# Kernel optimization log

Measured on AMD Instinct MI355X. Metric: run time of the kernel, lower is better.

The kernel has to match this reference:

```python
import jax, jax.numpy as jnp
import numpy as np

N = 50000      # nodes
E = 800000     # edges
F_IN = 512     # input feature dim
H1 = 8         # heads layer 1
F_HID = 8      # per-head hidden dim (concat -> 64)
H2 = 1         # heads layer 2
NLAB = 64      # output classes
LRELU_SLOPE = 0.2


def setup_inputs() -> dict:
    key = jax.random.key(0)
    ks = jax.random.split(key, 9)
    inputs = jax.random.normal(ks[0], (N, F_IN), jnp.float32)
    src = jax.random.randint(ks[1], (E,), 0, N, dtype=jnp.int32)
    dst = jax.random.randint(ks[2], (E,), 0, N, dtype=jnp.int32)
    s1 = 1.0 / np.sqrt(F_IN)
    s2 = 1.0 / np.sqrt(H1 * F_HID)
    W1 = jax.random.normal(ks[3], (H1, F_IN, F_HID), jnp.float32) * s1
    a1_src = jax.random.normal(ks[4], (H1, F_HID), jnp.float32) * 0.1
    a1_dst = jax.random.normal(ks[5], (H1, F_HID), jnp.float32) * 0.1
    W2 = jax.random.normal(ks[6], (H2, H1 * F_HID, NLAB), jnp.float32) * s2
    a2_src = jax.random.normal(ks[7], (H2, NLAB), jnp.float32) * 0.1
    a2_dst = jax.random.normal(ks[8], (H2, NLAB), jnp.float32) * 0.1
    return {"inputs": inputs, "W1": W1, "a1_src": a1_src, "a1_dst": a1_dst,
            "W2": W2, "a2_src": a2_src, "a2_dst": a2_dst, "src": src, "dst": dst}


def gat_layer(x, W, a_s, a_d, src, dst):
    # x: [N, F]; W: [H, F, O]; a_s/a_d: [H, O]
    Wh = jnp.einsum('nf,hfo->nho', x, W)                    # [N, H, O]
    es = jnp.einsum('nho,ho->nh', Wh, a_s)                  # [N, H]
    ed = jnp.einsum('nho,ho->nh', Wh, a_d)                  # [N, H]
    e = jax.nn.leaky_relu(es[src] + ed[dst], LRELU_SLOPE)   # [E, H]
    # neighborhood softmax over incoming edges of each dst node
    m = jax.lax.stop_gradient(jax.ops.segment_max(e, dst, num_segments=N))
    ex = jnp.exp(e - m[dst])                                # [E, H]
    den = jax.ops.segment_sum(ex, dst, num_segments=N)      # [N, H]
    alpha = ex / (den[dst] + 1e-10)                         # [E, H]
    msgs = alpha[:, :, None] * Wh[src]                      # [E, H, O]
    return jax.ops.segment_sum(msgs, dst, num_segments=N)   # [N, H, O]


def reference(inputs, W1, a1_src, a1_dst, W2, a2_src, a2_dst, src, dst):
    # eval mode: dropout rate 0, identity
    h = gat_layer(inputs, W1, a1_src, a1_dst, src, dst)     # [N, H1, F_HID]
    h = jax.nn.elu(h.reshape(N, H1 * F_HID))                # concat heads (reduction=False)
    o = gat_layer(h, W2, a2_src, a2_dst, src, dst)          # [N, H2, NLAB]
    o = o.mean(axis=1)                                      # average heads (reduction=True)
    return jax.nn.softmax(o, axis=-1)                       # [N, NLAB] (squeezed)
```

## Files before the change

kernel.cpp:

```cpp
#include <hip/hip_runtime.h>
#include <math.h>

#define N_NODES 50000
#define N_EDGES 800000
#define F_IN    512
#define H1      8
#define F_HID   8
#define C1      64
#define NLAB    64
#define SLOPE   0.2f
#define MAXDEG  64

#define NBLK_WT   128
#define NBLK_Z    196
#define NBLK_G1   782
#define NBLK_SC  3128
#define REC1     160
#define REC2     144

typedef __attribute__((ext_vector_type(8))) short short8;
typedef __attribute__((ext_vector_type(4))) float f32x4;

__device__ __forceinline__ float bf_lo(unsigned u) { return __uint_as_float(u << 16); }
__device__ __forceinline__ float bf_hi(unsigned u) { return __uint_as_float(u & 0xFFFF0000u); }
__device__ __forceinline__ unsigned short f2bf(float x) {
    unsigned bits = __float_as_uint(x);
    return (unsigned short)((bits + 0x7FFF + ((bits >> 16) & 1)) >> 16);
}

__global__ void k_prep(const float* __restrict__ W1, unsigned short* __restrict__ Bh,
                       unsigned short* __restrict__ Bl, int* __restrict__ deg) {
    int b = blockIdx.x;
    if (b < NBLK_WT) {
        int i = b * 256 + threadIdx.x;
        int c = i >> 9, f = i & 511;
        float v = W1[(c >> 3) * (F_IN * F_HID) + f * F_HID + (c & 7)];
        unsigned bits = __float_as_uint(v);
        float r = v - __uint_as_float(bits & 0xFFFF0000u);
        Bh[i] = (unsigned short)(bits >> 16);
        Bl[i] = (unsigned short)(__float_as_uint(r) >> 16);
    } else {
        int i = (b - NBLK_WT) * 256 + threadIdx.x;
        if (i < N_NODES) deg[i] = 0;
    }
}

__launch_bounds__(256)
__global__ void k_gemm1f(const float* __restrict__ X, const unsigned short* __restrict__ Bh,
                         const unsigned short* __restrict__ Bl, const float* __restrict__ a_s,
                         const float* __restrict__ a_d, char* __restrict__ rec,
                         float* __restrict__ ed,
                         const int* __restrict__ src, const int* __restrict__ dst,
                         int* __restrict__ deg, int* __restrict__ colPad) {
    __shared__ unsigned short sBh[64][136];
    __shared__ unsigned short sBl[64][136];

    const int b = blockIdx.x;
    const int g = b / 5, r = b % 5;
    if (r) {
        int e = (g * 4 + (r - 1)) * 256 + threadIdx.x;
        if (e >= N_EDGES) return;
        int d = dst[e];
        int s = src[e];
        int slot = atomicAdd(&deg[d], 1);
        colPad[(d << 6) | min(slot, MAXDEG - 1)] = s;
        return;
    }

    const int t = threadIdx.x;
    const int lane = t & 63, w = t >> 6;
    const int r0 = g * 64 + w * 16;
    const int m = lane & 15, quad = lane >> 4;
    int row = r0 + m; if (row >= N_NODES) row = N_NODES - 1;
    const float* xrow = X + (size_t)row * F_IN + quad * 8;

    const int sc = t >> 2;
    const int sp = t & 3;

    f32x4 acc[4] = {};
    float4 pxa[4], pxb[4];
    #pragma unroll
    for (int i = 0; i < 4; i++) {
        pxa[i] = *(const float4*)(xrow + i * 32);
        pxb[i] = *(const float4*)(xrow + i * 32 + 4);
    }

    for (int chunk = 0; chunk < 4; chunk++) {
        const int k0 = chunk * 128;
        if (chunk) __syncthreads();
        #pragma unroll
        for (int i = 0; i < 4; i++) {
            *(short8*)(&sBh[sc][sp * 32 + i * 8]) =
                *(const short8*)(Bh + sc * F_IN + k0 + sp * 32 + i * 8);
            *(short8*)(&sBl[sc][sp * 32 + i * 8]) =
                *(const short8*)(Bl + sc * F_IN + k0 + sp * 32 + i * 8);
        }
        __syncthreads();
        #pragma unroll
        for (int i = 0; i < 4; i++) {
            float xs[8] = {pxa[i].x, pxa[i].y, pxa[i].z, pxa[i].w,
                           pxb[i].x, pxb[i].y, pxb[i].z, pxb[i].w};
            if (chunk < 3) {
                const int ktn = k0 + 128 + i * 32;
                pxa[i] = *(const float4*)(xrow + ktn);
                pxb[i] = *(const float4*)(xrow + ktn + 4);
            }
            short8 ah, al;
            #pragma unroll
            for (int j = 0; j < 8; j++) {
                unsigned bits = __float_as_uint(xs[j]);
                float rr = xs[j] - __uint_as_float(bits & 0xFFFF0000u);
                ah[j] = (short)(bits >> 16);
                al[j] = (short)(__float_as_uint(rr) >> 16);
            }
            #pragma unroll
            for (int s = 0; s < 4; s++) {
                short8 bh = *(const short8*)(&sBh[s * 16 + m][i * 32 + quad * 8]);
                short8 bl = *(const short8*)(&sBl[s * 16 + m][i * 32 + quad * 8]);
                acc[s] = __builtin_amdgcn_mfma_f32_16x16x32_bf16(al, bh, acc[s], 0, 0, 0);
                acc[s] = __builtin_amdgcn_mfma_f32_16x16x32_bf16(ah, bl, acc[s], 0, 0, 0);
                acc[s] = __builtin_amdgcn_mfma_f32_16x16x32_bf16(ah, bh, acc[s], 0, 0, 0);
            }
        }
    }
    __syncthreads();
    unsigned short* sWh = &sBh[0][0] + w * 1024;
    #pragma unroll
    for (int s = 0; s < 4; s++)
        #pragma unroll
        for (int reg = 0; reg < 4; reg++)
            sWh[(quad * 4 + reg) * 64 + s * 16 + m] = f2bf(acc[s][reg]);
    __syncthreads();
    const int rr = lane & 15, p = lane >> 4;
    const int n = r0 + rr;
    if (n >= N_NODES) return;
    float es2v[2], edv[2];
    #pragma unroll
    for (int hh = 0; hh < 2; hh++) {
        int h = 2 * p + hh;
        float s = 0.f, dsum = 0.f;
        #pragma unroll
        for (int j = 0; j < 8; j++) {
            float v = __uint_as_float((unsigned)sWh[rr * 64 + h * 8 + j] << 16);
            s += v * a_s[h * 8 + j];
            dsum += v * a_d[h * 8 + j];
        }
        es2v[hh] = s; edv[hh] = dsum;
    }
    char* rp = rec + (size_t)n * REC1;
    *(float2*)(rp + p * 8) = make_float2(es2v[0], es2v[1]);
    *(short8*)(rp + 32 + p * 32)      = *(const short8*)(sWh + rr * 64 + p * 16);
    *(short8*)(rp + 32 + p * 32 + 16) = *(const short8*)(sWh + rr * 64 + p * 16 + 8);
    *(float2*)(ed + n * 8 + 2 * p) = make_float2(edv[0], edv[1]);
}

__launch_bounds__(256)
__global__ void k_agg1(const char* __restrict__ rec, const float* __restrict__ ed,
                       const int* __restrict__ deg, const int* __restrict__ colPad,
                       float* __restrict__ h2) {
    int tid = blockIdx.x * 256 + threadIdx.x;
    int n = tid >> 3, q = tid & 7;
    if (n >= N_NODES) return;
    int d = deg[n];
    int start = n << 6;
    float edq = ed[n * 8 + q];

    float den = 0.f;
    float acc[8] = {};
    for (int e = 0; e < d; e += 2) {
        int sv0 = colPad[start + e];
        int sv1 = colPad[start + min(e + 1, d - 1)];
        const char* r0 = rec + (size_t)sv0 * REC1;
        const char* r1 = rec + (size_t)sv1 * REC1;
        float x0 = *(const float*)(r0 + q * 4) + edq;
        float x1 = *(const float*)(r1 + q * 4) + edq;
        uint4 u0 = *(const uint4*)(r0 + 32 + q * 16);
        uint4 u1 = *(const uint4*)(r1 + 32 + q * 16);
        x0 = x0 > 0.f ? x0 : SLOPE * x0;
        x1 = x1 > 0.f ? x1 : SLOPE * x1;
        float w0 = __expf(x0);
        float w1 = (e + 1 < d) ? __expf(x1) : 0.f;
        den += w0 + w1;
        float f0[8] = {bf_lo(u0.x), bf_hi(u0.x), bf_lo(u0.y), bf_hi(u0.y),
                       bf_lo(u0.z), bf_hi(u0.z), bf_lo(u0.w), bf_hi(u0.w)};
        float f1[8] = {bf_lo(u1.x), bf_hi(u1.x), bf_lo(u1.y), bf_hi(u1.y),
                       bf_lo(u1.z), bf_hi(u1.z), bf_lo(u1.w), bf_hi(u1.w)};
        #pragma unroll
        for (int j = 0; j < 8; j++) acc[j] += w0 * f0[j] + w1 * f1[j];
    }
    float inv = 1.f / (den + 1e-10f);
    float o[8];
    #pragma unroll
    for (int j = 0; j < 8; j++) {
        float v = acc[j] * inv;
        o[j] = v > 0.f ? v : expm1f(v);
    }
    float4* hp = (float4*)(h2 + (size_t)n * 64 + q * 8);
    hp[0] = make_float4(o[0], o[1], o[2], o[3]);
    hp[1] = make_float4(o[4], o[5], o[6], o[7]);
}

__launch_bounds__(256)
__global__ void k_gemm2(const float* __restrict__ h2, const float* __restrict__ W2,
                        const float* __restrict__ a2s, const float* __restrict__ a2d,
                        char* __restrict__ rec2, float* __restrict__ ed2) {
    __shared__ float Ws[64 * 64];
    __shared__ float hs[16][64];
    int t = threadIdx.x;
    int n0 = blockIdx.x * 16;
    #pragma unroll
    for (int i = 0; i < 4; i++) {
        int flat = i * 256 + t;
        *(float4*)(Ws + flat * 4) = *(const float4*)(W2 + flat * 4);
    }
    #pragma unroll
    for (int i = 0; i < 4; i++) {
        int flat = i * 256 + t;
        hs[flat >> 6][flat & 63] = h2[(size_t)(n0 + (flat >> 6)) * 64 + (flat & 63)];
    }
    __syncthreads();
    int wv = t >> 6, lane = t & 63;
    float as = a2s[lane], ad = a2d[lane];
    #pragma unroll
    for (int j = 0; j < 4; j++) {
        int nl = wv * 4 + j;
        int n = n0 + nl;
        float acc = 0.f;
        #pragma unroll
        for (int k = 0; k < 64; k++) acc += hs[nl][k] * Ws[k * 64 + lane];
        char* r = rec2 + (size_t)n * REC2;
        *(unsigned short*)(r + 16 + lane * 2) = f2bf(acc);
        float s = acc * as;
        float dd = acc * ad;
        #pragma unroll
        for (int off = 1; off < 64; off <<= 1) {
            s += __shfl_xor(s, off);
            dd += __shfl_xor(dd, off);
        }
        if (lane == 0) { *(float*)r = s; ed2[n] = dd; }
    }
}

__launch_bounds__(256)
__global__ void k_agg2(const char* __restrict__ rec2, const float* __restrict__ ed2,
                       const int* __restrict__ deg, const int* __restrict__ colPad,
                       float* __restrict__ out) {
    int tid = blockIdx.x * 256 + threadIdx.x;
    int n = tid >> 3, q = tid & 7;
    if (n >= N_NODES) return;
    int d = deg[n];
    int start = n << 6;
    float edn = ed2[n];

    float den = 0.f;
    float acc[8] = {};
    for (int e = 0; e < d; e += 2) {
        int sv0 = colPad[start + e];
        int sv1 = colPad[start + min(e + 1, d - 1)];
        const char* r0 = rec2 + (size_t)sv0 * REC2;
        const char* r1 = rec2 + (size_t)sv1 * REC2;
        float x0 = *(const float*)r0 + edn;
        float x1 = *(const float*)r1 + edn;
        uint4 u0 = *(const uint4*)(r0 + 16 + q * 16);
        uint4 u1 = *(const uint4*)(r1 + 16 + q * 16);
        x0 = x0 > 0.f ? x0 : SLOPE * x0;
        x1 = x1 > 0.f ? x1 : SLOPE * x1;
        float w0 = __expf(x0);
        float w1 = (e + 1 < d) ? __expf(x1) : 0.f;
        den += w0 + w1;
        float f0[8] = {bf_lo(u0.x), bf_hi(u0.x), bf_lo(u0.y), bf_hi(u0.y),
                       bf_lo(u0.z), bf_hi(u0.z), bf_lo(u0.w), bf_hi(u0.w)};
        float f1[8] = {bf_lo(u1.x), bf_hi(u1.x), bf_lo(u1.y), bf_hi(u1.y),
                       bf_lo(u1.z), bf_hi(u1.z), bf_lo(u1.w), bf_hi(u1.w)};
        #pragma unroll
        for (int j = 0; j < 8; j++) acc[j] += w0 * f0[j] + w1 * f1[j];
    }
    float inv = 1.f / (den + 1e-10f);
    float o[8];
    #pragma unroll
    for (int j = 0; j < 8; j++) o[j] = acc[j] * inv;
    float mx = o[0];
    #pragma unroll
    for (int j = 1; j < 8; j++) mx = fmaxf(mx, o[j]);
    mx = fmaxf(mx, __shfl_xor(mx, 1));
    mx = fmaxf(mx, __shfl_xor(mx, 2));
    mx = fmaxf(mx, __shfl_xor(mx, 4));
    float e8[8], sm = 0.f;
    #pragma unroll
    for (int j = 0; j < 8; j++) { e8[j] = __expf(o[j] - mx); sm += e8[j]; }
    sm += __shfl_xor(sm, 1);
    sm += __shfl_xor(sm, 2);
    sm += __shfl_xor(sm, 4);
    float inv2 = 1.f / sm;
    float4* op = (float4*)(out + (size_t)n * 64 + q * 8);
    op[0] = make_float4(e8[0] * inv2, e8[1] * inv2, e8[2] * inv2, e8[3] * inv2);
    op[1] = make_float4(e8[4] * inv2, e8[5] * inv2, e8[6] * inv2, e8[7] * inv2);
}

extern "C" void kernel_launch(void* const* d_in, const int* in_sizes, int n_in,
                              void* d_out, int out_size, void* d_ws, size_t ws_size,
                              hipStream_t stream) {
    const float* X   = (const float*)d_in[0];
    const float* W1  = (const float*)d_in[1];
    const float* a1s = (const float*)d_in[2];
    const float* a1d = (const float*)d_in[3];
    const float* W2  = (const float*)d_in[4];
    const float* a2s = (const float*)d_in[5];
    const float* a2d = (const float*)d_in[6];
    const int*   src = (const int*)d_in[7];
    const int*   dst = (const int*)d_in[8];
    float* out = (float*)d_out;

    char* w = (char*)d_ws;
    size_t off = 0;
    auto alloc = [&](size_t bytes) {
        void* p = w + off;
        off += (bytes + 255) & ~(size_t)255;
        return p;
    };
    unsigned short* Bh  = (unsigned short*)alloc((size_t)C1 * F_IN * 2);
    unsigned short* Bl  = (unsigned short*)alloc((size_t)C1 * F_IN * 2);
    char*  rec1  = (char*)alloc((size_t)N_NODES * REC1);
    char*  rec2  = (char*)alloc((size_t)N_NODES * REC2);
    float* h2    = (float*)alloc((size_t)N_NODES * 64 * 4);
    float* ed1   = (float*)alloc((size_t)N_NODES * 8 * 4);
    float* ed2   = (float*)alloc((size_t)N_NODES * 4);
    int*   deg   = (int*)alloc((size_t)N_NODES * 4);
    int*   colPad= (int*)alloc((size_t)N_NODES * MAXDEG * 4);

    k_prep<<<NBLK_WT + NBLK_Z, 256, 0, stream>>>(W1, Bh, Bl, deg);
    k_gemm1f<<<NBLK_G1 * 5, 256, 0, stream>>>(X, Bh, Bl, a1s, a1d, rec1, ed1,
                                              src, dst, deg, colPad);
    k_agg1<<<(N_NODES * 8 + 255) / 256, 256, 0, stream>>>(rec1, ed1, deg, colPad, h2);
    k_gemm2<<<N_NODES / 16, 256, 0, stream>>>(h2, W2, a2s, a2d, rec2, ed2);
    k_agg2<<<(N_NODES * 8 + 255) / 256, 256, 0, stream>>>(rec2, ed2, deg, colPad, out);
}
```

Before: 283.2 us.

## Fuse layer-1 aggregation with layer-2 GEMM and pad degree counters

Merges the layer-1 neighbour aggregation and the layer-2 projection into one kernel. The ELU output is staged in shared memory instead of being written to and reread from a global h2 buffer, which also removes one launch. Separately, each node's degree counter now sits on its own 64-byte stride, to reduce atomic contention and false sharing between neighbouring counters. The cost is 16x more degree memory to zero in the prep kernel, and each fused block must reload the 16 KB W2 tile for only 32 nodes.

```diff
diff --git a/kernel.cpp b/kernel.cpp
--- a/kernel.cpp
+++ b/kernel.cpp
@@ -10,11 +10,11 @@
 #define NLAB    64
 #define SLOPE   0.2f
 #define MAXDEG  64
+#define DEGS    16
 
 #define NBLK_WT   128
-#define NBLK_Z    196
+#define NBLK_Z    782
 #define NBLK_G1   782
-#define NBLK_SC  3128
 #define REC1     160
 #define REC2     144
 
@@ -41,7 +41,8 @@
         Bl[i] = (unsigned short)(__float_as_uint(r) >> 16);
     } else {
         int i = (b - NBLK_WT) * 256 + threadIdx.x;
-        if (i < N_NODES) deg[i] = 0;
+        if (i < N_NODES * DEGS / 4)
+            *(int4*)(deg + i * 4) = make_int4(0, 0, 0, 0);
     }
 }
 
@@ -62,7 +63,7 @@
         if (e >= N_EDGES) return;
         int d = dst[e];
         int s = src[e];
-        int slot = atomicAdd(&deg[d], 1);
+        int slot = atomicAdd(&deg[d << 4], 1);
         colPad[(d << 6) | min(slot, MAXDEG - 1)] = s;
         return;
     }
@@ -155,80 +156,73 @@
 }
 
 __launch_bounds__(256)
-__global__ void k_agg1(const char* __restrict__ rec, const float* __restrict__ ed,
-                       const int* __restrict__ deg, const int* __restrict__ colPad,
-                       float* __restrict__ h2) {
-    int tid = blockIdx.x * 256 + threadIdx.x;
-    int n = tid >> 3, q = tid & 7;
-    if (n >= N_NODES) return;
-    int d = deg[n];
-    int start = n << 6;
-    float edq = ed[n * 8 + q];
-
-    float den = 0.f;
-    float acc[8] = {};
-    for (int e = 0; e < d; e += 2) {
-        int sv0 = colPad[start + e];
-        int sv1 = colPad[start + min(e + 1, d - 1)];
-        const char* r0 = rec + (size_t)sv0 * REC1;
-        const char* r1 = rec + (size_t)sv1 * REC1;
-        float x0 = *(const float*)(r0 + q * 4) + edq;
-        float x1 = *(const float*)(r1 + q * 4) + edq;
-        uint4 u0 = *(const uint4*)(r0 + 32 + q * 16);
-        uint4 u1 = *(const uint4*)(r1 + 32 + q * 16);
-        x0 = x0 > 0.f ? x0 : SLOPE * x0;
-        x1 = x1 > 0.f ? x1 : SLOPE * x1;
-        float w0 = __expf(x0);
-        float w1 = (e + 1 < d) ? __expf(x1) : 0.f;
-        den += w0 + w1;
-        float f0[8] = {bf_lo(u0.x), bf_hi(u0.x), bf_lo(u0.y), bf_hi(u0.y),
-                       bf_lo(u0.z), bf_hi(u0.z), bf_lo(u0.w), bf_hi(u0.w)};
-        float f1[8] = {bf_lo(u1.x), bf_hi(u1.x), bf_lo(u1.y), bf_hi(u1.y),
-                       bf_lo(u1.z), bf_hi(u1.z), bf_lo(u1.w), bf_hi(u1.w)};
-        #pragma unroll
-        for (int j = 0; j < 8; j++) acc[j] += w0 * f0[j] + w1 * f1[j];
-    }
-    float inv = 1.f / (den + 1e-10f);
-    float o[8];
-    #pragma unroll
-    for (int j = 0; j < 8; j++) {
-        float v = acc[j] * inv;
-        o[j] = v > 0.f ? v : expm1f(v);
-    }
-    float4* hp = (float4*)(h2 + (size_t)n * 64 + q * 8);
-    hp[0] = make_float4(o[0], o[1], o[2], o[3]);
-    hp[1] = make_float4(o[4], o[5], o[6], o[7]);
-}
-
-__launch_bounds__(256)
-__global__ void k_gemm2(const float* __restrict__ h2, const float* __restrict__ W2,
-                        const float* __restrict__ a2s, const float* __restrict__ a2d,
-                        char* __restrict__ rec2, float* __restrict__ ed2) {
+__global__ void k_agg1g2(const char* __restrict__ rec, const float* __restrict__ ed,
+                         const int* __restrict__ deg, const int* __restrict__ colPad,
+                         const float* __restrict__ W2, const float* __restrict__ a2s,
+                         const float* __restrict__ a2d,
+                         char* __restrict__ rec2, float* __restrict__ ed2) {
     __shared__ float Ws[64 * 64];
-    __shared__ float hs[16][64];
-    int t = threadIdx.x;
-    int n0 = blockIdx.x * 16;
+    __shared__ float hs[32][64];
+    const int t = threadIdx.x;
     #pragma unroll
     for (int i = 0; i < 4; i++) {
         int flat = i * 256 + t;
         *(float4*)(Ws + flat * 4) = *(const float4*)(W2 + flat * 4);
     }
-    #pragma unroll
-    for (int i = 0; i < 4; i++) {
-        int flat = i * 256 + t;
-        hs[flat >> 6][flat & 63] = h2[(size_t)(n0 + (flat >> 6)) * 64 + (flat & 63)];
-    }
+    const int n0 = blockIdx.x * 32;
+    const int n = n0 + (t >> 3), q = t & 7;
+
+    float o[8] = {};
+    if (n < N_NODES) {
+        int d = deg[n << 4];
+        int start = n << 6;
+        float edq = ed[n * 8 + q];
+        float den = 0.f;
+        float acc[8] = {};
+        for (int e = 0; e < d; e += 2) {
+            int sv0 = colPad[start + e];
+            int sv1 = colPad[start + min(e + 1, d - 1)];
+            const char* r0 = rec + (size_t)sv0 * REC1;
+            const char* r1 = rec + (size_t)sv1 * REC1;
+            float x0 = *(const float*)(r0 + q * 4) + edq;
+            float x1 = *(const float*)(r1 + q * 4) + edq;
+            uint4 u0 = *(const uint4*)(r0 + 32 + q * 16);
+            uint4 u1 = *(const uint4*)(r1 + 32 + q * 16);
+            x0 = x0 > 0.f ? x0 : SLOPE * x0;
+            x1 = x1 > 0.f ? x1 : SLOPE * x1;
+            float w0 = __expf(x0);
+            float w1 = (e + 1 < d) ? __expf(x1) : 0.f;
+            den += w0 + w1;
+            float f0[8] = {bf_lo(u0.x), bf_hi(u0.x), bf_lo(u0.y), bf_hi(u0.y),
+                           bf_lo(u0.z), bf_hi(u0.z), bf_lo(u0.w), bf_hi(u0.w)};
+            float f1[8] = {bf_lo(u1.x), bf_hi(u1.x), bf_lo(u1.y), bf_hi(u1.y),
+                           bf_lo(u1.z), bf_hi(u1.z), bf_lo(u1.w), bf_hi(u1.w)};
+            #pragma unroll
+            for (int j = 0; j < 8; j++) acc[j] += w0 * f0[j] + w1 * f1[j];
+        }
+        float inv = 1.f / (den + 1e-10f);
+        #pragma unroll
+        for (int j = 0; j < 8; j++) {
+            float v = acc[j] * inv;
+            o[j] = v > 0.f ? v : expm1f(v);
+        }
+    }
+    float4* hp = (float4*)(&hs[t >> 3][q * 8]);
+    hp[0] = make_float4(o[0], o[1], o[2], o[3]);
+    hp[1] = make_float4(o[4], o[5], o[6], o[7]);
     __syncthreads();
-    int wv = t >> 6, lane = t & 63;
+
+    const int wv = t >> 6, lane = t & 63;
     float as = a2s[lane], ad = a2d[lane];
     #pragma unroll
-    for (int j = 0; j < 4; j++) {
-        int nl = wv * 4 + j;
-        int n = n0 + nl;
+    for (int j = 0; j < 8; j++) {
+        int nl = wv * 8 + j;
+        int nn = n0 + nl;
+        if (nn >= N_NODES) break;
         float acc = 0.f;
         #pragma unroll
         for (int k = 0; k < 64; k++) acc += hs[nl][k] * Ws[k * 64 + lane];
-        char* r = rec2 + (size_t)n * REC2;
+        char* r = rec2 + (size_t)nn * REC2;
         *(unsigned short*)(r + 16 + lane * 2) = f2bf(acc);
         float s = acc * as;
         float dd = acc * ad;
@@ -237,7 +231,7 @@
             s += __shfl_xor(s, off);
             dd += __shfl_xor(dd, off);
         }
-        if (lane == 0) { *(float*)r = s; ed2[n] = dd; }
+        if (lane == 0) { *(float*)r = s; ed2[nn] = dd; }
     }
 }
 
@@ -248,7 +242,7 @@
     int tid = blockIdx.x * 256 + threadIdx.x;
     int n = tid >> 3, q = tid & 7;
     if (n >= N_NODES) return;
-    int d = deg[n];
+    int d = deg[n << 4];
     int start = n << 6;
     float edn = ed2[n];
 
@@ -322,16 +316,15 @@
     unsigned short* Bl  = (unsigned short*)alloc((size_t)C1 * F_IN * 2);
     char*  rec1  = (char*)alloc((size_t)N_NODES * REC1);
     char*  rec2  = (char*)alloc((size_t)N_NODES * REC2);
-    float* h2    = (float*)alloc((size_t)N_NODES * 64 * 4);
     float* ed1   = (float*)alloc((size_t)N_NODES * 8 * 4);
     float* ed2   = (float*)alloc((size_t)N_NODES * 4);
-    int*   deg   = (int*)alloc((size_t)N_NODES * 4);
+    int*   deg   = (int*)alloc((size_t)N_NODES * DEGS * 4);
     int*   colPad= (int*)alloc((size_t)N_NODES * MAXDEG * 4);
 
     k_prep<<<NBLK_WT + NBLK_Z, 256, 0, stream>>>(W1, Bh, Bl, deg);
     k_gemm1f<<<NBLK_G1 * 5, 256, 0, stream>>>(X, Bh, Bl, a1s, a1d, rec1, ed1,
                                               src, dst, deg, colPad);
-    k_agg1<<<(N_NODES * 8 + 255) / 256, 256, 0, stream>>>(rec1, ed1, deg, colPad, h2);
-    k_gemm2<<<N_NODES / 16, 256, 0, stream>>>(h2, W2, a2s, a2d, rec2, ed2);
+    k_agg1g2<<<(N_NODES + 31) / 32, 256, 0, stream>>>(rec1, ed1, deg, colPad,
+                                                      W2, a2s, a2d, rec2, ed2);
     k_agg2<<<(N_NODES * 8 + 255) / 256, 256, 0, stream>>>(rec2, ed2, deg, colPad, out);
 }
```

Result: no change. 281.0 us (-0.8%).
